# Kernel optimization log

Measured on AMD Instinct MI355X. Metric: run time of the kernel, lower is better.

The kernel has to match this reference:

```python
import jax, jax.numpy as jnp
import numpy as np

B, S, H = 2, 256, 2048
HK, HV, DK, DV, K = 16, 32, 128, 128, 4
KEY_DIM = HK * DK          # 2048
VAL_DIM = HV * DV          # 4096
CONV_DIM = 2 * KEY_DIM + VAL_DIM  # 8192
EPS = 1e-6


def setup_inputs() -> dict:
    key = jax.random.key(0)
    ks = jax.random.split(key, 10)
    s = 0.02
    return {
        "hidden_states": jax.random.normal(ks[0], (B, S, H), jnp.float32),
        "conv_state": jnp.zeros((B, CONV_DIM, K - 1), jnp.float32),
        "recurrent_state": jnp.zeros((B, HV, DK, DV), jnp.float32),
        "context_lengths": jnp.full((B,), S, jnp.int32),
        "W_qkv": jax.random.normal(ks[1], (H, CONV_DIM), jnp.float32) * s,
        "W_z": jax.random.normal(ks[2], (H, VAL_DIM), jnp.float32) * s,
        "W_b": jax.random.normal(ks[3], (H, HV), jnp.float32) * s,
        "W_a": jax.random.normal(ks[4], (H, HV), jnp.float32) * s,
        "conv_w": jax.random.normal(ks[5], (CONV_DIM, K), jnp.float32) * 0.1,
        "conv_b": jnp.zeros((CONV_DIM,), jnp.float32),
        "A_log": jax.random.normal(ks[6], (HV,), jnp.float32) * 0.1,
        "dt_bias": jnp.zeros((HV,), jnp.float32),
        "norm_w": jnp.ones((DV,), jnp.float32),
        "W_out": jax.random.normal(ks[7], (VAL_DIM, H), jnp.float32) * s,
    }


def _l2norm(x):
    return x * jax.lax.rsqrt(jnp.sum(x * x, axis=-1, keepdims=True) + EPS)


def reference(hidden_states, conv_state, recurrent_state, context_lengths,
              W_qkv, W_z, W_b, W_a, conv_w, conv_b, A_log, dt_bias,
              norm_w, W_out):
    # input projections
    mixed = hidden_states @ W_qkv            # [B,S,CONV_DIM]
    z = hidden_states @ W_z                  # [B,S,VAL_DIM]
    b = hidden_states @ W_b                  # [B,S,HV]
    a = hidden_states @ W_a                  # [B,S,HV]

    # stateful causal depthwise conv1d (kernel K, padding K-1)
    x_pad = jnp.concatenate([jnp.swapaxes(conv_state, 1, 2), mixed], axis=1)  # [B,S+K-1,C]
    conv_out = conv_b + sum(x_pad[:, j:j + S, :] * conv_w[:, j] for j in range(K))
    conv_state_out = jnp.swapaxes(x_pad[:, S:, :], 1, 2)  # last K-1 raw inputs [B,C,K-1]
    mixed = jax.nn.silu(conv_out)

    q, k, v = jnp.split(mixed, [KEY_DIM, 2 * KEY_DIM], axis=-1)
    q = _l2norm(q.reshape(B, S, HK, DK)) * (DK ** -0.5)
    k = _l2norm(k.reshape(B, S, HK, DK))
    v = v.reshape(B, S, HV, DV)
    # GQA-style repeat of key/query heads to value heads
    rep = HV // HK
    q = jnp.repeat(q, rep, axis=2)           # [B,S,HV,DK]
    k = jnp.repeat(k, rep, axis=2)

    # gating: log-decay g and write strength beta
    g = -jnp.exp(A_log) * jax.nn.softplus(a + dt_bias)  # [B,S,HV]
    beta = jax.nn.sigmoid(b)                            # [B,S,HV]

    # time-major for scan
    qs = jnp.swapaxes(q, 0, 1)   # [S,B,HV,DK]
    ks_ = jnp.swapaxes(k, 0, 1)
    vs = jnp.swapaxes(v, 0, 1)   # [S,B,HV,DV]
    gs = jnp.swapaxes(g, 0, 1)   # [S,B,HV]
    bs = jnp.swapaxes(beta, 0, 1)
    mask = jnp.arange(S)[:, None] < context_lengths[None, :]  # [S,B]

    def step(Sst, inp):
        qt, kt, vt, gt, bt, mt = inp
        Sd = Sst * jnp.exp(gt)[..., None, None]                # decay
        kv = jnp.einsum('bhk,bhkv->bhv', kt, Sd)               # prediction
        delta = (vt - kv) * bt[..., None]                      # delta-rule update
        Snew = Sd + jnp.einsum('bhk,bhv->bhkv', kt, delta)
        ot = jnp.einsum('bhk,bhkv->bhv', qt, Snew)
        Snew = jnp.where(mt[:, None, None, None], Snew, Sst)
        ot = jnp.where(mt[:, None, None], ot, 0.0)
        return Snew, ot

    Sfin, outs = jax.lax.scan(step, recurrent_state, (qs, ks_, vs, gs, bs, mask))
    o = jnp.swapaxes(outs, 0, 1)  # [B,S,HV,DV]

    # gated RMSNorm over value head dim
    o = o * jax.lax.rsqrt(jnp.mean(o * o, axis=-1, keepdims=True) + EPS) * norm_w
    o = o * jax.nn.silu(z.reshape(B, S, HV, DV))
    output = o.reshape(B, S, VAL_DIM) @ W_out
    return output, conv_state_out, Sfin
```

## Files before the change

### kernel.cpp

```cpp
#include <hip/hip_runtime.h>
#include <hip/hip_bf16.h>

#define BB     2
#define SEQ    256
#define HH     2048
#define HKc    16
#define HVc    32
#define DKc    128
#define DVc    128
#define KC     4
#define KEYD   2048
#define VALD   4096
#define CONVD  8192
#define MM     (BB*SEQ)
#define EPSf   1e-6f

typedef __attribute__((ext_vector_type(8))) short short8;
typedef __attribute__((ext_vector_type(4))) short short4v;
typedef __attribute__((ext_vector_type(4))) float floatx4;

__device__ __forceinline__ short f2bf(float f) {
  union { float f; unsigned u; } v; v.f = f;
  unsigned r = v.u + 0x7fffu + ((v.u >> 16) & 1u);
  return (short)(r >> 16);
}

__global__ __launch_bounds__(256) void zerof_kernel(float* __restrict__ p) {
  float4 z; z.x = 0.f; z.y = 0.f; z.z = 0.f; z.w = 0.f;
  *(float4*)&p[(size_t)(blockIdx.x * 256 + threadIdx.x) * 4] = z;
}

__global__ __launch_bounds__(256) void trconv_kernel(
    const float* __restrict__ W, short* __restrict__ Wt, int K, int N) {
  __shared__ float ls[64][33];
  const int n0 = blockIdx.x * 32;
  const int k0 = blockIdx.y * 64;
  const int t = threadIdx.x;
#pragma unroll
  for (int it = 0; it < 2; ++it) {
    const int kr = (t >> 3) + it * 32;
    const int c4 = (t & 7) * 4;
    const float4 f = *(const float4*)&W[(size_t)(k0 + kr) * N + n0 + c4];
    ls[kr][c4] = f.x; ls[kr][c4 + 1] = f.y; ls[kr][c4 + 2] = f.z; ls[kr][c4 + 3] = f.w;
  }
  __syncthreads();
  const int r = t >> 3;
  const int kc = (t & 7) * 8;
  short8 s;
#pragma unroll
  for (int j = 0; j < 8; ++j) s[j] = f2bf(ls[kc + j][r]);
  *(short8*)&Wt[(size_t)(n0 + r) * K + k0 + kc] = s;
}

__global__ __launch_bounds__(256) void f2bf_kernel(
    const float* __restrict__ in, short* __restrict__ out) {
  const int i = blockIdx.x * 256 + threadIdx.x;
  const float4 a = *(const float4*)&in[(size_t)i * 8];
  const float4 b = *(const float4*)&in[(size_t)i * 8 + 4];
  short8 s;
  s[0] = f2bf(a.x); s[1] = f2bf(a.y); s[2] = f2bf(a.z); s[3] = f2bf(a.w);
  s[4] = f2bf(b.x); s[5] = f2bf(b.y); s[6] = f2bf(b.z); s[7] = f2bf(b.w);
  *(short8*)&out[(size_t)i * 8] = s;
}

#define PADs 40
__global__ __launch_bounds__(256) void gemm_bf16(
    const short* __restrict__ A, const short* __restrict__ Bt,
    float* __restrict__ C, int M, int N, int Kd, int lda, int klen, int atom) {
  __shared__ short As[64 * PADs];
  __shared__ short Bs[128 * PADs];
  const int tid = threadIdx.x;
  const int wave = tid >> 6, lane = tid & 63;
  const int wm = (wave >> 1) * 32, wn = (wave & 1) * 64;
  const int bm = blockIdx.y * 64, bn = blockIdx.x * 128;
  const int koff = blockIdx.z * klen;
  floatx4 acc[2][4] = {};
  const int sa_m = tid >> 2;
  const int sa_k = (tid & 3) * 8;
  const int fm = lane & 15, fq = (lane >> 4) * 8;
  const short* Ap  = A  + (size_t)(bm + sa_m) * lda + koff + sa_k;
  const short* Bp0 = Bt + (size_t)(bn + sa_m) * Kd + koff + sa_k;
  const short* Bp1 = Bt + (size_t)(bn + 64 + sa_m) * Kd + koff + sa_k;
  short8 pa  = *(const short8*)(Ap);
  short8 pb0 = *(const short8*)(Bp0);
  short8 pb1 = *(const short8*)(Bp1);
  for (int k0 = 0; k0 < klen; k0 += 32) {
    *(short8*)&As[sa_m * PADs + sa_k] = pa;
    *(short8*)&Bs[sa_m * PADs + sa_k] = pb0;
    *(short8*)&Bs[(64 + sa_m) * PADs + sa_k] = pb1;
    __syncthreads();
    if (k0 + 32 < klen) {
      pa  = *(const short8*)(Ap + k0 + 32);
      pb0 = *(const short8*)(Bp0 + k0 + 32);
      pb1 = *(const short8*)(Bp1 + k0 + 32);
    }
    short8 af[2], bfr[4];
#pragma unroll
    for (int i = 0; i < 2; ++i)
      af[i] = *(const short8*)&As[(wm + i * 16 + fm) * PADs + fq];
#pragma unroll
    for (int j = 0; j < 4; ++j)
      bfr[j] = *(const short8*)&Bs[(wn + j * 16 + fm) * PADs + fq];
#pragma unroll
    for (int i = 0; i < 2; ++i)
#pragma unroll
      for (int j = 0; j < 4; ++j)
        acc[i][j] = __builtin_amdgcn_mfma_f32_16x16x32_bf16(af[i], bfr[j], acc[i][j], 0, 0, 0);
    __syncthreads();
  }
  const int cn = lane & 15, cr0 = (lane >> 4) * 4;
  if (atom) {
#pragma unroll
    for (int i = 0; i < 2; ++i)
#pragma unroll
      for (int j = 0; j < 4; ++j)
#pragma unroll
        for (int r = 0; r < 4; ++r)
          atomicAdd(&C[(size_t)(bm + wm + i * 16 + cr0 + r) * N + bn + wn + j * 16 + cn],
                    acc[i][j][r]);
  } else {
#pragma unroll
    for (int i = 0; i < 2; ++i)
#pragma unroll
      for (int j = 0; j < 4; ++j)
#pragma unroll
        for (int r = 0; r < 4; ++r)
          C[(size_t)(bm + wm + i * 16 + cr0 + r) * N + bn + wn + j * 16 + cn] = acc[i][j][r];
  }
}

__global__ __launch_bounds__(256) void proj_ab_kernel(
    const float* __restrict__ hs, const float* __restrict__ Wb,
    const float* __restrict__ Wa, const float* __restrict__ A_log,
    const float* __restrict__ dt_bias, float* __restrict__ g_out,
    float* __restrict__ beta_out) {
  __shared__ float xs[HH];
  __shared__ float part[4][64];
  const int row = blockIdx.x;
  const int t = threadIdx.x;
  for (int i = t; i < HH; i += 256) xs[i] = hs[(size_t)row * HH + i];
  __syncthreads();
  const int j = t & 63;
  const int kc = t >> 6;
  const float* W = (j < 32) ? Wb : Wa;
  const int jj = j & 31;
  float p = 0.f;
  const int k0 = kc * 512;
#pragma unroll 8
  for (int k = k0; k < k0 + 512; ++k) p += xs[k] * W[k * 32 + jj];
  part[kc][j] = p;
  __syncthreads();
  if (t < 64) {
    float dot = part[0][t] + part[1][t] + part[2][t] + part[3][t];
    if (t < 32) {
      beta_out[row * HVc + t] = 1.f / (1.f + expf(-dot));
    } else {
      int h = t - 32;
      float x = dot + dt_bias[h];
      float sp = (x > 20.f) ? x : log1pf(expf(x));
      g_out[row * HVc + h] = -expf(A_log[h]) * sp;
    }
  }
}

#define CCH 16
__global__ __launch_bounds__(256) void conv_par_kernel(
    const float* __restrict__ mixed, const float* __restrict__ conv_state,
    const float* __restrict__ conv_w, const float* __restrict__ conv_b,
    float* __restrict__ cs) {
  const int c = blockIdx.x * 256 + threadIdx.x;
  const int s0 = blockIdx.y * CCH;
  const int b = blockIdx.z;
  const float4 w4 = *(const float4*)&conv_w[c * KC];
  const float bias = conv_b[c];
  float r0, r1, r2;
  if (s0 == 0) {
    size_t sb = (size_t)(b * CONVD + c) * (KC - 1);
    r0 = conv_state[sb + 0]; r1 = conv_state[sb + 1]; r2 = conv_state[sb + 2];
  } else {
    r0 = mixed[((size_t)(b * SEQ + s0 - 3)) * CONVD + c];
    r1 = mixed[((size_t)(b * SEQ + s0 - 2)) * CONVD + c];
    r2 = mixed[((size_t)(b * SEQ + s0 - 1)) * CONVD + c];
  }
#pragma unroll
  for (int s = s0; s < s0 + CCH; ++s) {
    size_t off = ((size_t)(b * SEQ + s)) * CONVD + c;
    float x = mixed[off];
    float acc = bias + r0 * w4.x + r1 * w4.y + r2 * w4.z + x * w4.w;
    cs[off] = acc / (1.f + expf(-acc));
    r0 = r1; r1 = r2; r2 = x;
  }
}

__global__ __launch_bounds__(256) void conv_state_out_kernel(
    const float* __restrict__ mixed, float* __restrict__ out2) {
  int idx = blockIdx.x * 256 + threadIdx.x;
  int t = idx % (KC - 1);
  int c = (idx / (KC - 1)) & (CONVD - 1);
  int b = idx / ((KC - 1) * CONVD);
  out2[idx] = mixed[((size_t)(b * SEQ + SEQ - (KC - 1) + t)) * CONVD + c];
}

__global__ __launch_bounds__(64) void l2norm_kernel(float* __restrict__ cs) {
  int bx = blockIdx.x;
  int which = bx & 1;
  int head = (bx >> 1) & 15;
  int row = bx >> 5;
  int lane = threadIdx.x;
  size_t base = (size_t)row * CONVD + (size_t)which * KEYD + head * DKc;
  float v0 = cs[base + lane];
  float v1 = cs[base + lane + 64];
  float ss = v0 * v0 + v1 * v1;
#pragma unroll
  for (int m = 1; m < 64; m <<= 1) ss += __shfl_xor(ss, m, 64);
  float rn = rsqrtf(ss + EPSf);
  if (!which) rn *= 0.08838834764831845f;
  cs[base + lane] = v0 * rn;
  cs[base + lane + 64] = v1 * rn;
}

#define SCH 8
__global__ __launch_bounds__(64, 2) void scan_kernel(
    const float* __restrict__ cs, const float* __restrict__ g_in,
    const float* __restrict__ beta_in, const float* __restrict__ rs0,
    const int* __restrict__ ctx, float* __restrict__ obuf,
    float* __restrict__ sftmp) {
  const int vg = blockIdx.x, h = blockIdx.y, b = blockIdx.z;
  const int bh = b * HVc + h;
  const int lane = threadIdx.x;
  const int kg = lane >> 2;
  const int c4 = lane & 3;
  const int col = vg * 4 + c4;
  const int khead = h >> 1;
  __shared__ float kl[2][SCH * 128];
  __shared__ float ql[2][SCH * 128];
  __shared__ float vl[2][SCH * 4];
  __shared__ float egl[2][SCH];
  __shared__ float btl[2][SCH];
  float S[8];
#pragma unroll
  for (int i = 0; i < 8; ++i)
    S[i] = rs0[((size_t)bh * DKc + kg * 8 + i) * DVc + col];
  const int cl = ctx[b];
  const size_t qgo = (size_t)khead * DKc;
  const size_t kgo = KEYD + (size_t)khead * DKc;
  const size_t vG = 2 * KEYD + (size_t)h * DVc + vg * 4;
  const size_t obase = ((size_t)bh * 32 + vg) * (SEQ * 4);
  const int r0g = b * SEQ;
  const int kg8 = kg * 8;
  float4 kreg[4], qreg[4], vreg;
  float egr = 0.f, btr = 0.f;
#pragma unroll
  for (int it = 0; it < 4; ++it) {
    int idx = it * 64 + lane, s = idx >> 5, d4 = idx & 31;
    const float* rp = cs + (size_t)(r0g + s) * CONVD;
    kreg[it] = *(const float4*)(rp + kgo + d4 * 4);
    qreg[it] = *(const float4*)(rp + qgo + d4 * 4);
  }
  if (lane < 8)       vreg = *(const float4*)(cs + (size_t)(r0g + lane) * CONVD + vG);
  else if (lane < 16) egr = expf(g_in[(r0g + lane - 8) * HVc + h]);
  else if (lane < 24) btr = beta_in[(r0g + lane - 16) * HVc + h];
#pragma unroll
  for (int it = 0; it < 4; ++it) {
    int idx = it * 64 + lane, s = idx >> 5, d4 = idx & 31;
    *(float4*)&kl[0][s * 128 + d4 * 4] = kreg[it];
    *(float4*)&ql[0][s * 128 + d4 * 4] = qreg[it];
  }
  if (lane < 8)       *(float4*)&vl[0][lane * 4] = vreg;
  else if (lane < 16) egl[0][lane - 8] = egr;
  else if (lane < 24) btl[0][lane - 16] = btr;

  const int NCH = SEQ / SCH;
  for (int c = 0; c < NCH; ++c) {
    const int buf = c & 1;
    if (c + 1 < NCH) {
      const int r1 = r0g + (c + 1) * SCH;
#pragma unroll
      for (int it = 0; it < 4; ++it) {
        int idx = it * 64 + lane, s = idx >> 5, d4 = idx & 31;
        const float* rp = cs + (size_t)(r1 + s) * CONVD;
        kreg[it] = *(const float4*)(rp + kgo + d4 * 4);
        qreg[it] = *(const float4*)(rp + qgo + d4 * 4);
      }
      if (lane < 8)       vreg = *(const float4*)(cs + (size_t)(r1 + lane) * CONVD + vG);
      else if (lane < 16) egr = expf(g_in[(r1 + lane - 8) * HVc + h]);
      else if (lane < 24) btr = beta_in[(r1 + lane - 16) * HVc + h];
    }
#pragma unroll
    for (int s = 0; s < SCH; ++s) {
      const int sg = c * SCH + s;
      const float eg = egl[buf][s], bt = btl[buf][s];
      const float vv = vl[buf][s * 4 + c4];
      const float4* k4 = (const float4*)&kl[buf][s * 128 + kg8];
      const float4* q4 = (const float4*)&ql[buf][s * 128 + kg8];
      if (sg < cl) {
        const float4 kk0 = k4[0], kk1 = k4[1];
        float a0, a1, a2, a3;
        S[0] *= eg; a0 = kk0.x * S[0];
        S[1] *= eg; a1 = kk0.y * S[1];
        S[2] *= eg; a2 = kk0.z * S[2];
        S[3] *= eg; a3 = kk0.w * S[3];
        S[4] *= eg; a0 += kk1.x * S[4];
        S[5] *= eg; a1 += kk1.y * S[5];
        S[6] *= eg; a2 += kk1.z * S[6];
        S[7] *= eg; a3 += kk1.w * S[7];
        float p = (a0 + a1) + (a2 + a3);
        p += __shfl_xor(p, 4, 64);
        p += __shfl_xor(p, 8, 64);
        p += __shfl_xor(p, 16, 64);
        p += __shfl_xor(p, 32, 64);
        const float delta = (vv - p) * bt;
        const float4 qq0 = q4[0], qq1 = q4[1];
        float o0, o1, o2, o3;
        S[0] += kk0.x * delta; o0 = qq0.x * S[0];
        S[1] += kk0.y * delta; o1 = qq0.y * S[1];
        S[2] += kk0.z * delta; o2 = qq0.z * S[2];
        S[3] += kk0.w * delta; o3 = qq0.w * S[3];
        S[4] += kk1.x * delta; o0 += qq1.x * S[4];
        S[5] += kk1.y * delta; o1 += qq1.y * S[5];
        S[6] += kk1.z * delta; o2 += qq1.z * S[6];
        S[7] += kk1.w * delta; o3 += qq1.w * S[7];
        float o = (o0 + o1) + (o2 + o3);
        o += __shfl_xor(o, 4, 64);
        o += __shfl_xor(o, 8, 64);
        o += __shfl_xor(o, 16, 64);
        o += __shfl_xor(o, 32, 64);
        if (kg == 0) obuf[obase + sg * 4 + c4] = o;
      } else {
        if (kg == 0) obuf[obase + sg * 4 + c4] = 0.f;
      }
    }
    if (c + 1 < NCH) {
      const int nb = buf ^ 1;
#pragma unroll
      for (int it = 0; it < 4; ++it) {
        int idx = it * 64 + lane, s = idx >> 5, d4 = idx & 31;
        *(float4*)&kl[nb][s * 128 + d4 * 4] = kreg[it];
        *(float4*)&ql[nb][s * 128 + d4 * 4] = qreg[it];
      }
      if (lane < 8)       *(float4*)&vl[nb][lane * 4] = vreg;
      else if (lane < 16) egl[nb][lane - 8] = egr;
      else if (lane < 24) btl[nb][lane - 16] = btr;
    }
  }
  const size_t sb = (((size_t)bh * 32 + vg) * DKc + kg8) * 4 + c4;
#pragma unroll
  for (int i = 0; i < 8; ++i)
    sftmp[sb + i * 4] = S[i];
}

__global__ __launch_bounds__(128) void sfin_tr_kernel(
    const float* __restrict__ sftmp, float* __restrict__ out_sf) {
  const int dk = blockIdx.x;
  const int bh = blockIdx.y;
  const int dv = threadIdx.x;
  out_sf[((size_t)bh * DKc + dk) * DVc + dv] =
      sftmp[(((size_t)bh * 32 + (dv >> 2)) * DKc + dk) * 4 + (dv & 3)];
}

__global__ __launch_bounds__(64) void normgate_kernel(
    const float* __restrict__ obuf, const float* __restrict__ zbuf,
    const float* __restrict__ norm_w, short* __restrict__ o16) {
  int bx = blockIdx.x;
  int h = bx & 31;
  int row = bx >> 5;
  int b = row >> 8;
  int s = row & (SEQ - 1);
  int lane = threadIdx.x;
  size_t ob = ((size_t)(b * HVc + h) * 32 + (lane >> 2)) * (SEQ * 4) + s * 4 + (lane & 3);
  size_t zb = (size_t)row * VALD + h * DVc;
  float o0 = obuf[ob];
  float o1 = obuf[ob + 16 * (SEQ * 4)];
  float ss = o0 * o0 + o1 * o1;
#pragma unroll
  for (int m = 1; m < 64; m <<= 1) ss += __shfl_xor(ss, m, 64);
  float rms = rsqrtf(ss * (1.f / 128.f) + EPSf);
  float z0 = zbuf[zb + lane];
  float z1 = zbuf[zb + lane + 64];
  o16[zb + lane]      = f2bf(o0 * rms * norm_w[lane]      * (z0 / (1.f + expf(-z0))));
  o16[zb + lane + 64] = f2bf(o1 * rms * norm_w[lane + 64] * (z1 / (1.f + expf(-z1))));
}

extern "C" void kernel_launch(void* const* d_in, const int* in_sizes, int n_in,
                              void* d_out, int out_size, void* d_ws, size_t ws_size,
                              hipStream_t stream) {
  const float* hs        = (const float*)d_in[0];
  const float* conv_st   = (const float*)d_in[1];
  const float* rec_st    = (const float*)d_in[2];
  const int*   ctx       = (const int*)d_in[3];
  const float* W_qkv     = (const float*)d_in[4];
  const float* W_z       = (const float*)d_in[5];
  const float* W_b       = (const float*)d_in[6];
  const float* W_a       = (const float*)d_in[7];
  const float* conv_w    = (const float*)d_in[8];
  const float* conv_b    = (const float*)d_in[9];
  const float* A_log     = (const float*)d_in[10];
  const float* dt_bias   = (const float*)d_in[11];
  const float* norm_w    = (const float*)d_in[12];
  const float* W_out     = (const float*)d_in[13];

  float* out0   = (float*)d_out;
  float* out_cv = out0 + (size_t)MM * HH;
  float* out_sf = out_cv + (size_t)BB * CONVD * (KC - 1);

  char*  base  = (char*)d_ws;
  float* mixed = (float*)base;
  char*  wtB   = base + (size_t)MM * CONVD * 4;
  short* wt    = (short*)wtB;
  float* cs    = (float*)wtB;
  float* zbuf  = (float*)(wtB + (size_t)MM * CONVD * 4);
  float* gbuf  = (float*)(wtB + (size_t)CONVD * HH * 2);
  float* betab = gbuf + (size_t)MM * HVc;
  short* hs16  = (short*)(betab + (size_t)MM * HVc);
  short* o16   = hs16 + (size_t)MM * HH;
  float* obuf  = mixed;
  float* sftmp = mixed + (size_t)MM * VALD;

  f2bf_kernel<<<(MM * HH / 8) / 256, 256, 0, stream>>>(hs, hs16);
  trconv_kernel<<<dim3(CONVD / 32, HH / 64), 256, 0, stream>>>(W_qkv, wt, HH, CONVD);
  zerof_kernel<<<(MM * CONVD / 4) / 256, 256, 0, stream>>>(mixed);
  gemm_bf16<<<dim3(CONVD / 128, MM / 64, 2), 256, 0, stream>>>(
      hs16, wt, mixed, MM, CONVD, HH, HH, HH / 2, 1);
  trconv_kernel<<<dim3(VALD / 32, HH / 64), 256, 0, stream>>>(W_z, wt, HH, VALD);
  zerof_kernel<<<(MM * VALD / 4) / 256, 256, 0, stream>>>(zbuf);
  gemm_bf16<<<dim3(VALD / 128, MM / 64, 2), 256, 0, stream>>>(
      hs16, wt, zbuf, MM, VALD, HH, HH, HH / 2, 1);
  proj_ab_kernel<<<MM, 256, 0, stream>>>(hs, W_b, W_a, A_log, dt_bias, gbuf, betab);
  conv_par_kernel<<<dim3(CONVD / 256, SEQ / CCH, BB), 256, 0, stream>>>(
      mixed, conv_st, conv_w, conv_b, cs);
  conv_state_out_kernel<<<(BB * CONVD * (KC - 1)) / 256, 256, 0, stream>>>(mixed, out_cv);
  l2norm_kernel<<<MM * HKc * 2, 64, 0, stream>>>(cs);
  scan_kernel<<<dim3(32, HVc, BB), 64, 0, stream>>>(cs, gbuf, betab, rec_st, ctx, obuf, sftmp);
  sfin_tr_kernel<<<dim3(DKc, BB * HVc), 128, 0, stream>>>(sftmp, out_sf);
  normgate_kernel<<<MM * HVc, 64, 0, stream>>>(obuf, zbuf, norm_w, o16);
  trconv_kernel<<<dim3(HH / 32, VALD / 64), 256, 0, stream>>>(W_out, wt, VALD, HH);
  zerof_kernel<<<(MM * HH / 4) / 256, 256, 0, stream>>>(out0);
  gemm_bf16<<<dim3(HH / 128, MM / 64, 4), 256, 0, stream>>>(
      o16, wt, out0, MM, HH, VALD, VALD, VALD / 4, 1);
}
```

Measured before the change: 517.9 us.

## Split scan state across more blocks and deepen GEMM K-tile to 64

The recurrent scan kernel now gives each 64-lane block 2 value columns instead of 4, with 4 state rows per lane instead of 8. This doubles the grid to 4096 blocks and shortens each lane's serial dependency chain, at the cost of an extra shuffle-reduction step and twice the redundant k/q loads per block. The obuf, sftmp and normgate/sfin indexing are updated to match the new layout. Separately, the bf16 GEMM stages a K-slice of 64 per iteration instead of 32, halving the number of barriers and loop trips in exchange for more LDS and registers per block.

After: 561.5 us. 8.4% more time.

```diff
diff --git a/kernel.cpp b/kernel.cpp
--- a/kernel.cpp
+++ b/kernel.cpp
@@ -63,49 +63,63 @@
   *(short8*)&out[(size_t)i * 8] = s;
 }
 
-#define PADs 40
+#define PAD2 72
 __global__ __launch_bounds__(256) void gemm_bf16(
     const short* __restrict__ A, const short* __restrict__ Bt,
     float* __restrict__ C, int M, int N, int Kd, int lda, int klen, int atom) {
-  __shared__ short As[64 * PADs];
-  __shared__ short Bs[128 * PADs];
+  __shared__ short As[64 * PAD2];
+  __shared__ short Bs[128 * PAD2];
   const int tid = threadIdx.x;
   const int wave = tid >> 6, lane = tid & 63;
   const int wm = (wave >> 1) * 32, wn = (wave & 1) * 64;
   const int bm = blockIdx.y * 64, bn = blockIdx.x * 128;
   const int koff = blockIdx.z * klen;
   floatx4 acc[2][4] = {};
-  const int sa_m = tid >> 2;
-  const int sa_k = (tid & 3) * 8;
+  const int sr = tid >> 3;
+  const int skc = (tid & 7) * 8;
   const int fm = lane & 15, fq = (lane >> 4) * 8;
-  const short* Ap  = A  + (size_t)(bm + sa_m) * lda + koff + sa_k;
-  const short* Bp0 = Bt + (size_t)(bn + sa_m) * Kd + koff + sa_k;
-  const short* Bp1 = Bt + (size_t)(bn + 64 + sa_m) * Kd + koff + sa_k;
-  short8 pa  = *(const short8*)(Ap);
-  short8 pb0 = *(const short8*)(Bp0);
-  short8 pb1 = *(const short8*)(Bp1);
-  for (int k0 = 0; k0 < klen; k0 += 32) {
-    *(short8*)&As[sa_m * PADs + sa_k] = pa;
-    *(short8*)&Bs[sa_m * PADs + sa_k] = pb0;
-    *(short8*)&Bs[(64 + sa_m) * PADs + sa_k] = pb1;
+  const short* Ap = A  + koff + skc;
+  const short* Bp = Bt + koff + skc;
+  short8 pa[2], pb[4];
+#pragma unroll
+  for (int it = 0; it < 2; ++it)
+    pa[it] = *(const short8*)(Ap + (size_t)(bm + sr + it * 32) * lda);
+#pragma unroll
+  for (int it = 0; it < 4; ++it)
+    pb[it] = *(const short8*)(Bp + (size_t)(bn + sr + it * 32) * Kd);
+  for (int k0 = 0; k0 < klen; k0 += 64) {
+#pragma unroll
+    for (int it = 0; it < 2; ++it)
+      *(short8*)&As[(sr + it * 32) * PAD2 + skc] = pa[it];
+#pragma unroll
+    for (int it = 0; it < 4; ++it)
+      *(short8*)&Bs[(sr + it * 32) * PAD2 + skc] = pb[it];
     __syncthreads();
-    if (k0 + 32 < klen) {
-      pa  = *(const short8*)(Ap + k0 + 32);
-      pb0 = *(const short8*)(Bp0 + k0 + 32);
-      pb1 = *(const short8*)(Bp1 + k0 + 32);
-    }
-    short8 af[2], bfr[4];
-#pragma unroll
-    for (int i = 0; i < 2; ++i)
-      af[i] = *(const short8*)&As[(wm + i * 16 + fm) * PADs + fq];
-#pragma unroll
-    for (int j = 0; j < 4; ++j)
-      bfr[j] = *(const short8*)&Bs[(wn + j * 16 + fm) * PADs + fq];
-#pragma unroll
-    for (int i = 0; i < 2; ++i)
+    if (k0 + 64 < klen) {
+#pragma unroll
+      for (int it = 0; it < 2; ++it)
+        pa[it] = *(const short8*)(Ap + (size_t)(bm + sr + it * 32) * lda + k0 + 64);
+#pragma unroll
+      for (int it = 0; it < 4; ++it)
+        pb[it] = *(const short8*)(Bp + (size_t)(bn + sr + it * 32) * Kd + k0 + 64);
+    }
+    short8 af[2][2], bfr[2][4];
+#pragma unroll
+    for (int hh = 0; hh < 2; ++hh) {
+#pragma unroll
+      for (int i = 0; i < 2; ++i)
+        af[hh][i] = *(const short8*)&As[(wm + i * 16 + fm) * PAD2 + hh * 32 + fq];
 #pragma unroll
       for (int j = 0; j < 4; ++j)
-        acc[i][j] = __builtin_amdgcn_mfma_f32_16x16x32_bf16(af[i], bfr[j], acc[i][j], 0, 0, 0);
+        bfr[hh][j] = *(const short8*)&Bs[(wn + j * 16 + fm) * PAD2 + hh * 32 + fq];
+    }
+#pragma unroll
+    for (int hh = 0; hh < 2; ++hh)
+#pragma unroll
+      for (int i = 0; i < 2; ++i)
+#pragma unroll
+        for (int j = 0; j < 4; ++j)
+          acc[i][j] = __builtin_amdgcn_mfma_f32_16x16x32_bf16(af[hh][i], bfr[hh][j], acc[i][j], 0, 0, 0);
     __syncthreads();
   }
   const int cn = lane & 15, cr0 = (lane >> 4) * 4;
@@ -219,8 +233,8 @@
   cs[base + lane + 64] = v1 * rn;
 }
 
-#define SCH 8
-__global__ __launch_bounds__(64, 2) void scan_kernel(
+#define SCH 4
+__global__ __launch_bounds__(64, 4) void scan_kernel(
     const float* __restrict__ cs, const float* __restrict__ g_in,
     const float* __restrict__ beta_in, const float* __restrict__ rs0,
     const int* __restrict__ ctx, float* __restrict__ obuf,
@@ -228,47 +242,47 @@
   const int vg = blockIdx.x, h = blockIdx.y, b = blockIdx.z;
   const int bh = b * HVc + h;
   const int lane = threadIdx.x;
-  const int kg = lane >> 2;
-  const int c4 = lane & 3;
-  const int col = vg * 4 + c4;
+  const int kg = lane >> 1;
+  const int c2 = lane & 1;
+  const int col = vg * 2 + c2;
   const int khead = h >> 1;
   __shared__ float kl[2][SCH * 128];
   __shared__ float ql[2][SCH * 128];
-  __shared__ float vl[2][SCH * 4];
+  __shared__ float vl[2][SCH * 2];
   __shared__ float egl[2][SCH];
   __shared__ float btl[2][SCH];
-  float S[8];
-#pragma unroll
-  for (int i = 0; i < 8; ++i)
-    S[i] = rs0[((size_t)bh * DKc + kg * 8 + i) * DVc + col];
+  float S[4];
+#pragma unroll
+  for (int i = 0; i < 4; ++i)
+    S[i] = rs0[((size_t)bh * DKc + kg * 4 + i) * DVc + col];
   const int cl = ctx[b];
   const size_t qgo = (size_t)khead * DKc;
   const size_t kgo = KEYD + (size_t)khead * DKc;
-  const size_t vG = 2 * KEYD + (size_t)h * DVc + vg * 4;
-  const size_t obase = ((size_t)bh * 32 + vg) * (SEQ * 4);
+  const size_t vG = 2 * KEYD + (size_t)h * DVc + vg * 2;
+  const size_t obase = ((size_t)bh * 64 + vg) * (SEQ * 2);
   const int r0g = b * SEQ;
-  const int kg8 = kg * 8;
-  float4 kreg[4], qreg[4], vreg;
-  float egr = 0.f, btr = 0.f;
-#pragma unroll
-  for (int it = 0; it < 4; ++it) {
+  const int kg4 = kg * 4;
+  float4 kreg[2], qreg[2];
+  float vreg = 0.f, egr = 0.f, btr = 0.f;
+#pragma unroll
+  for (int it = 0; it < 2; ++it) {
     int idx = it * 64 + lane, s = idx >> 5, d4 = idx & 31;
     const float* rp = cs + (size_t)(r0g + s) * CONVD;
     kreg[it] = *(const float4*)(rp + kgo + d4 * 4);
     qreg[it] = *(const float4*)(rp + qgo + d4 * 4);
   }
-  if (lane < 8)       vreg = *(const float4*)(cs + (size_t)(r0g + lane) * CONVD + vG);
-  else if (lane < 16) egr = expf(g_in[(r0g + lane - 8) * HVc + h]);
-  else if (lane < 24) btr = beta_in[(r0g + lane - 16) * HVc + h];
-#pragma unroll
-  for (int it = 0; it < 4; ++it) {
+  if (lane < 8)       vreg = cs[(size_t)(r0g + (lane >> 1)) * CONVD + vG + (lane & 1)];
+  else if (lane < 12) egr = expf(g_in[(r0g + lane - 8) * HVc + h]);
+  else if (lane < 16) btr = beta_in[(r0g + lane - 12) * HVc + h];
+#pragma unroll
+  for (int it = 0; it < 2; ++it) {
     int idx = it * 64 + lane, s = idx >> 5, d4 = idx & 31;
     *(float4*)&kl[0][s * 128 + d4 * 4] = kreg[it];
     *(float4*)&ql[0][s * 128 + d4 * 4] = qreg[it];
   }
-  if (lane < 8)       *(float4*)&vl[0][lane * 4] = vreg;
-  else if (lane < 16) egl[0][lane - 8] = egr;
-  else if (lane < 24) btl[0][lane - 16] = btr;
+  if (lane < 8)       vl[0][lane] = vreg;
+  else if (lane < 12) egl[0][lane - 8] = egr;
+  else if (lane < 16) btl[0][lane - 12] = btr;
 
   const int NCH = SEQ / SCH;
   for (int c = 0; c < NCH; ++c) {
@@ -276,77 +290,69 @@
     if (c + 1 < NCH) {
       const int r1 = r0g + (c + 1) * SCH;
 #pragma unroll
-      for (int it = 0; it < 4; ++it) {
+      for (int it = 0; it < 2; ++it) {
         int idx = it * 64 + lane, s = idx >> 5, d4 = idx & 31;
         const float* rp = cs + (size_t)(r1 + s) * CONVD;
         kreg[it] = *(const float4*)(rp + kgo + d4 * 4);
         qreg[it] = *(const float4*)(rp + qgo + d4 * 4);
       }
-      if (lane < 8)       vreg = *(const float4*)(cs + (size_t)(r1 + lane) * CONVD + vG);
-      else if (lane < 16) egr = expf(g_in[(r1 + lane - 8) * HVc + h]);
-      else if (lane < 24) btr = beta_in[(r1 + lane - 16) * HVc + h];
+      if (lane < 8)       vreg = cs[(size_t)(r1 + (lane >> 1)) * CONVD + vG + (lane & 1)];
+      else if (lane < 12) egr = expf(g_in[(r1 + lane - 8) * HVc + h]);
+      else if (lane < 16) btr = beta_in[(r1 + lane - 12) * HVc + h];
     }
 #pragma unroll
     for (int s = 0; s < SCH; ++s) {
       const int sg = c * SCH + s;
       const float eg = egl[buf][s], bt = btl[buf][s];
-      const float vv = vl[buf][s * 4 + c4];
-      const float4* k4 = (const float4*)&kl[buf][s * 128 + kg8];
-      const float4* q4 = (const float4*)&ql[buf][s * 128 + kg8];
+      const float vv = vl[buf][s * 2 + c2];
+      const float4 kk = *(const float4*)&kl[buf][s * 128 + kg4];
+      const float4 qq = *(const float4*)&ql[buf][s * 128 + kg4];
       if (sg < cl) {
-        const float4 kk0 = k4[0], kk1 = k4[1];
         float a0, a1, a2, a3;
-        S[0] *= eg; a0 = kk0.x * S[0];
-        S[1] *= eg; a1 = kk0.y * S[1];
-        S[2] *= eg; a2 = kk0.z * S[2];
-        S[3] *= eg; a3 = kk0.w * S[3];
-        S[4] *= eg; a0 += kk1.x * S[4];
-        S[5] *= eg; a1 += kk1.y * S[5];
-        S[6] *= eg; a2 += kk1.z * S[6];
-        S[7] *= eg; a3 += kk1.w * S[7];
+        S[0] *= eg; a0 = kk.x * S[0];
+        S[1] *= eg; a1 = kk.y * S[1];
+        S[2] *= eg; a2 = kk.z * S[2];
+        S[3] *= eg; a3 = kk.w * S[3];
         float p = (a0 + a1) + (a2 + a3);
+        p += __shfl_xor(p, 2, 64);
         p += __shfl_xor(p, 4, 64);
         p += __shfl_xor(p, 8, 64);
         p += __shfl_xor(p, 16, 64);
         p += __shfl_xor(p, 32, 64);
         const float delta = (vv - p) * bt;
-        const float4 qq0 = q4[0], qq1 = q4[1];
         float o0, o1, o2, o3;
-        S[0] += kk0.x * delta; o0 = qq0.x * S[0];
-        S[1] += kk0.y * delta; o1 = qq0.y * S[1];
-        S[2] += kk0.z * delta; o2 = qq0.z * S[2];
-        S[3] += kk0.w * delta; o3 = qq0.w * S[3];
-        S[4] += kk1.x * delta; o0 += qq1.x * S[4];
-        S[5] += kk1.y * delta; o1 += qq1.y * S[5];
-        S[6] += kk1.z * delta; o2 += qq1.z * S[6];
-        S[7] += kk1.w * delta; o3 += qq1.w * S[7];
+        S[0] += kk.x * delta; o0 = qq.x * S[0];
+        S[1] += kk.y * delta; o1 = qq.y * S[1];
+        S[2] += kk.z * delta; o2 = qq.z * S[2];
+        S[3] += kk.w * delta; o3 = qq.w * S[3];
         float o = (o0 + o1) + (o2 + o3);
+        o += __shfl_xor(o, 2, 64);
         o += __shfl_xor(o, 4, 64);
         o += __shfl_xor(o, 8, 64);
         o += __shfl_xor(o, 16, 64);
         o += __shfl_xor(o, 32, 64);
-        if (kg == 0) obuf[obase + sg * 4 + c4] = o;
+        if (kg == 0) obuf[obase + sg * 2 + c2] = o;
       } else {
-        if (kg == 0) obuf[obase + sg * 4 + c4] = 0.f;
+        if (kg == 0) obuf[obase + sg * 2 + c2] = 0.f;
       }
     }
     if (c + 1 < NCH) {
       const int nb = buf ^ 1;
 #pragma unroll
-      for (int it = 0; it < 4; ++it) {
+      for (int it = 0; it < 2; ++it) {
         int idx = it * 64 + lane, s = idx >> 5, d4 = idx & 31;
         *(float4*)&kl[nb][s * 128 + d4 * 4] = kreg[it];
         *(float4*)&ql[nb][s * 128 + d4 * 4] = qreg[it];
       }
-      if (lane < 8)       *(float4*)&vl[nb][lane * 4] = vreg;
-      else if (lane < 16) egl[nb][lane - 8] = egr;
-      else if (lane < 24) btl[nb][lane - 16] = btr;
-    }
-  }
-  const size_t sb = (((size_t)bh * 32 + vg) * DKc + kg8) * 4 + c4;
-#pragma unroll
-  for (int i = 0; i < 8; ++i)
-    sftmp[sb + i * 4] = S[i];
+      if (lane < 8)       vl[nb][lane] = vreg;
+      else if (lane < 12) egl[nb][lane - 8] = egr;
+      else if (lane < 16) btl[nb][lane - 12] = btr;
+    }
+  }
+  const size_t sb = (((size_t)bh * 64 + vg) * DKc + kg4) * 2 + c2;
+#pragma unroll
+  for (int i = 0; i < 4; ++i)
+    sftmp[sb + i * 2] = S[i];
 }
 
 __global__ __launch_bounds__(128) void sfin_tr_kernel(
@@ -355,7 +361,7 @@
   const int bh = blockIdx.y;
   const int dv = threadIdx.x;
   out_sf[((size_t)bh * DKc + dk) * DVc + dv] =
-      sftmp[(((size_t)bh * 32 + (dv >> 2)) * DKc + dk) * 4 + (dv & 3)];
+      sftmp[(((size_t)bh * 64 + (dv >> 1)) * DKc + dk) * 2 + (dv & 1)];
 }
 
 __global__ __launch_bounds__(64) void normgate_kernel(
@@ -367,10 +373,10 @@
   int b = row >> 8;
   int s = row & (SEQ - 1);
   int lane = threadIdx.x;
-  size_t ob = ((size_t)(b * HVc + h) * 32 + (lane >> 2)) * (SEQ * 4) + s * 4 + (lane & 3);
+  size_t ob = ((size_t)(b * HVc + h) * 64 + (lane >> 1)) * (SEQ * 2) + s * 2 + (lane & 1);
   size_t zb = (size_t)row * VALD + h * DVc;
   float o0 = obuf[ob];
-  float o1 = obuf[ob + 16 * (SEQ * 4)];
+  float o1 = obuf[ob + 32 * (SEQ * 2)];
   float ss = o0 * o0 + o1 * o1;
 #pragma unroll
   for (int m = 1; m < 64; m <<= 1) ss += __shfl_xor(ss, m, 64);
@@ -430,7 +436,7 @@
       mixed, conv_st, conv_w, conv_b, cs);
   conv_state_out_kernel<<<(BB * CONVD * (KC - 1)) / 256, 256, 0, stream>>>(mixed, out_cv);
   l2norm_kernel<<<MM * HKc * 2, 64, 0, stream>>>(cs);
-  scan_kernel<<<dim3(32, HVc, BB), 64, 0, stream>>>(cs, gbuf, betab, rec_st, ctx, obuf, sftmp);
+  scan_kernel<<<dim3(64, HVc, BB), 64, 0, stream>>>(cs, gbuf, betab, rec_st, ctx, obuf, sftmp);
   sfin_tr_kernel<<<dim3(DKc, BB * HVc), 128, 0, stream>>>(sftmp, out_sf);
   normgate_kernel<<<MM * HVc, 64, 0, stream>>>(obuf, zbuf, norm_w, o16);
   trconv_kernel<<<dim3(HH / 32, VALD / 64), 256, 0, stream>>>(W_out, wt, VALD, HH);
```

## Deepen GEMM K-tile to 64 and overlap output reduction with next-step prediction

Applied to the files above, without the earlier changes.

The bf16 GEMM now stages 64-wide K tiles in shared memory, with padded rows, and issues two MFMA half-steps per barrier pair. This halves the number of synchronizations and gives each wave more loads in flight. In the delta-rule scan, the per-step output reduction is deferred by one step so its cross-lane shuffles interleave with the next step's prediction shuffles, shortening the serial dependency chain. Masked timesteps become branch-free through neutral decay and beta values. The GEMM change uses more shared memory and registers, which may lower occupancy.

New measurement: 530.7 us. 1.02x slower.

```diff
diff --git a/kernel.cpp b/kernel.cpp
--- a/kernel.cpp
+++ b/kernel.cpp
@@ -63,49 +63,63 @@
   *(short8*)&out[(size_t)i * 8] = s;
 }
 
-#define PADs 40
+#define PAD2 72
 __global__ __launch_bounds__(256) void gemm_bf16(
     const short* __restrict__ A, const short* __restrict__ Bt,
     float* __restrict__ C, int M, int N, int Kd, int lda, int klen, int atom) {
-  __shared__ short As[64 * PADs];
-  __shared__ short Bs[128 * PADs];
+  __shared__ short As[64 * PAD2];
+  __shared__ short Bs[128 * PAD2];
   const int tid = threadIdx.x;
   const int wave = tid >> 6, lane = tid & 63;
   const int wm = (wave >> 1) * 32, wn = (wave & 1) * 64;
   const int bm = blockIdx.y * 64, bn = blockIdx.x * 128;
   const int koff = blockIdx.z * klen;
   floatx4 acc[2][4] = {};
-  const int sa_m = tid >> 2;
-  const int sa_k = (tid & 3) * 8;
+  const int sr = tid >> 3;
+  const int skc = (tid & 7) * 8;
   const int fm = lane & 15, fq = (lane >> 4) * 8;
-  const short* Ap  = A  + (size_t)(bm + sa_m) * lda + koff + sa_k;
-  const short* Bp0 = Bt + (size_t)(bn + sa_m) * Kd + koff + sa_k;
-  const short* Bp1 = Bt + (size_t)(bn + 64 + sa_m) * Kd + koff + sa_k;
-  short8 pa  = *(const short8*)(Ap);
-  short8 pb0 = *(const short8*)(Bp0);
-  short8 pb1 = *(const short8*)(Bp1);
-  for (int k0 = 0; k0 < klen; k0 += 32) {
-    *(short8*)&As[sa_m * PADs + sa_k] = pa;
-    *(short8*)&Bs[sa_m * PADs + sa_k] = pb0;
-    *(short8*)&Bs[(64 + sa_m) * PADs + sa_k] = pb1;
+  const short* Ap = A  + koff + skc;
+  const short* Bp = Bt + koff + skc;
+  short8 pa[2], pb[4];
+#pragma unroll
+  for (int it = 0; it < 2; ++it)
+    pa[it] = *(const short8*)(Ap + (size_t)(bm + sr + it * 32) * lda);
+#pragma unroll
+  for (int it = 0; it < 4; ++it)
+    pb[it] = *(const short8*)(Bp + (size_t)(bn + sr + it * 32) * Kd);
+  for (int k0 = 0; k0 < klen; k0 += 64) {
+#pragma unroll
+    for (int it = 0; it < 2; ++it)
+      *(short8*)&As[(sr + it * 32) * PAD2 + skc] = pa[it];
+#pragma unroll
+    for (int it = 0; it < 4; ++it)
+      *(short8*)&Bs[(sr + it * 32) * PAD2 + skc] = pb[it];
     __syncthreads();
-    if (k0 + 32 < klen) {
-      pa  = *(const short8*)(Ap + k0 + 32);
-      pb0 = *(const short8*)(Bp0 + k0 + 32);
-      pb1 = *(const short8*)(Bp1 + k0 + 32);
-    }
-    short8 af[2], bfr[4];
-#pragma unroll
-    for (int i = 0; i < 2; ++i)
-      af[i] = *(const short8*)&As[(wm + i * 16 + fm) * PADs + fq];
-#pragma unroll
-    for (int j = 0; j < 4; ++j)
-      bfr[j] = *(const short8*)&Bs[(wn + j * 16 + fm) * PADs + fq];
-#pragma unroll
-    for (int i = 0; i < 2; ++i)
+    if (k0 + 64 < klen) {
+#pragma unroll
+      for (int it = 0; it < 2; ++it)
+        pa[it] = *(const short8*)(Ap + (size_t)(bm + sr + it * 32) * lda + k0 + 64);
+#pragma unroll
+      for (int it = 0; it < 4; ++it)
+        pb[it] = *(const short8*)(Bp + (size_t)(bn + sr + it * 32) * Kd + k0 + 64);
+    }
+    short8 af[2][2], bfr[2][4];
+#pragma unroll
+    for (int hh = 0; hh < 2; ++hh) {
+#pragma unroll
+      for (int i = 0; i < 2; ++i)
+        af[hh][i] = *(const short8*)&As[(wm + i * 16 + fm) * PAD2 + hh * 32 + fq];
 #pragma unroll
       for (int j = 0; j < 4; ++j)
-        acc[i][j] = __builtin_amdgcn_mfma_f32_16x16x32_bf16(af[i], bfr[j], acc[i][j], 0, 0, 0);
+        bfr[hh][j] = *(const short8*)&Bs[(wn + j * 16 + fm) * PAD2 + hh * 32 + fq];
+    }
+#pragma unroll
+    for (int hh = 0; hh < 2; ++hh)
+#pragma unroll
+      for (int i = 0; i < 2; ++i)
+#pragma unroll
+        for (int j = 0; j < 4; ++j)
+          acc[i][j] = __builtin_amdgcn_mfma_f32_16x16x32_bf16(af[hh][i], bfr[hh][j], acc[i][j], 0, 0, 0);
     __syncthreads();
   }
   const int cn = lane & 15, cr0 = (lane >> 4) * 4;
@@ -270,6 +284,7 @@
   else if (lane < 16) egl[0][lane - 8] = egr;
   else if (lane < 24) btl[0][lane - 16] = btr;
 
+  float opend = 0.f;
   const int NCH = SEQ / SCH;
   for (int c = 0; c < NCH; ++c) {
     const int buf = c & 1;
@@ -289,46 +304,41 @@
 #pragma unroll
     for (int s = 0; s < SCH; ++s) {
       const int sg = c * SCH + s;
-      const float eg = egl[buf][s], bt = btl[buf][s];
+      const bool act = sg < cl;
+      const float eg = act ? egl[buf][s] : 1.f;
+      const float bt = act ? btl[buf][s] : 0.f;
       const float vv = vl[buf][s * 4 + c4];
       const float4* k4 = (const float4*)&kl[buf][s * 128 + kg8];
       const float4* q4 = (const float4*)&ql[buf][s * 128 + kg8];
-      if (sg < cl) {
-        const float4 kk0 = k4[0], kk1 = k4[1];
-        float a0, a1, a2, a3;
-        S[0] *= eg; a0 = kk0.x * S[0];
-        S[1] *= eg; a1 = kk0.y * S[1];
-        S[2] *= eg; a2 = kk0.z * S[2];
-        S[3] *= eg; a3 = kk0.w * S[3];
-        S[4] *= eg; a0 += kk1.x * S[4];
-        S[5] *= eg; a1 += kk1.y * S[5];
-        S[6] *= eg; a2 += kk1.z * S[6];
-        S[7] *= eg; a3 += kk1.w * S[7];
-        float p = (a0 + a1) + (a2 + a3);
-        p += __shfl_xor(p, 4, 64);
-        p += __shfl_xor(p, 8, 64);
-        p += __shfl_xor(p, 16, 64);
-        p += __shfl_xor(p, 32, 64);
-        const float delta = (vv - p) * bt;
-        const float4 qq0 = q4[0], qq1 = q4[1];
-        float o0, o1, o2, o3;
-        S[0] += kk0.x * delta; o0 = qq0.x * S[0];
-        S[1] += kk0.y * delta; o1 = qq0.y * S[1];
-        S[2] += kk0.z * delta; o2 = qq0.z * S[2];
-        S[3] += kk0.w * delta; o3 = qq0.w * S[3];
-        S[4] += kk1.x * delta; o0 += qq1.x * S[4];
-        S[5] += kk1.y * delta; o1 += qq1.y * S[5];
-        S[6] += kk1.z * delta; o2 += qq1.z * S[6];
-        S[7] += kk1.w * delta; o3 += qq1.w * S[7];
-        float o = (o0 + o1) + (o2 + o3);
-        o += __shfl_xor(o, 4, 64);
-        o += __shfl_xor(o, 8, 64);
-        o += __shfl_xor(o, 16, 64);
-        o += __shfl_xor(o, 32, 64);
-        if (kg == 0) obuf[obase + sg * 4 + c4] = o;
-      } else {
-        if (kg == 0) obuf[obase + sg * 4 + c4] = 0.f;
-      }
+      const float4 kk0 = k4[0], kk1 = k4[1];
+      float a0, a1, a2, a3;
+      S[0] *= eg; a0 = kk0.x * S[0];
+      S[1] *= eg; a1 = kk0.y * S[1];
+      S[2] *= eg; a2 = kk0.z * S[2];
+      S[3] *= eg; a3 = kk0.w * S[3];
+      S[4] *= eg; a0 += kk1.x * S[4];
+      S[5] *= eg; a1 += kk1.y * S[5];
+      S[6] *= eg; a2 += kk1.z * S[6];
+      S[7] *= eg; a3 += kk1.w * S[7];
+      float p = (a0 + a1) + (a2 + a3);
+      float oo = opend;
+      p  += __shfl_xor(p, 4, 64);   oo += __shfl_xor(oo, 4, 64);
+      p  += __shfl_xor(p, 8, 64);   oo += __shfl_xor(oo, 8, 64);
+      p  += __shfl_xor(p, 16, 64);  oo += __shfl_xor(oo, 16, 64);
+      p  += __shfl_xor(p, 32, 64);  oo += __shfl_xor(oo, 32, 64);
+      if (kg == 0 && sg > 0) obuf[obase + (sg - 1) * 4 + c4] = oo;
+      const float delta = (vv - p) * bt;
+      const float4 qq0 = q4[0], qq1 = q4[1];
+      float o0, o1, o2, o3;
+      S[0] += kk0.x * delta; o0 = qq0.x * S[0];
+      S[1] += kk0.y * delta; o1 = qq0.y * S[1];
+      S[2] += kk0.z * delta; o2 = qq0.z * S[2];
+      S[3] += kk0.w * delta; o3 = qq0.w * S[3];
+      S[4] += kk1.x * delta; o0 += qq1.x * S[4];
+      S[5] += kk1.y * delta; o1 += qq1.y * S[5];
+      S[6] += kk1.z * delta; o2 += qq1.z * S[6];
+      S[7] += kk1.w * delta; o3 += qq1.w * S[7];
+      opend = act ? (o0 + o1) + (o2 + o3) : 0.f;
     }
     if (c + 1 < NCH) {
       const int nb = buf ^ 1;
@@ -342,6 +352,14 @@
       else if (lane < 16) egl[nb][lane - 8] = egr;
       else if (lane < 24) btl[nb][lane - 16] = btr;
     }
+  }
+  {
+    float oo = opend;
+    oo += __shfl_xor(oo, 4, 64);
+    oo += __shfl_xor(oo, 8, 64);
+    oo += __shfl_xor(oo, 16, 64);
+    oo += __shfl_xor(oo, 32, 64);
+    if (kg == 0) obuf[obase + (SEQ - 1) * 4 + c4] = oo;
   }
   const size_t sb = (((size_t)bh * 32 + vg) * DKc + kg8) * 4 + c4;
 #pragma unroll
```
